# Kernel tuning notes

Hardware: AMD Instinct MI355X
Metric: run time of the kernel (lower is better)

The kernel has to match this reference:

```python
import jax, jax.numpy as jnp
import numpy as np

B, H, N, D = 4, 16, 4096, 64
M = 266  # nb_features = int(D * ln(D))
KERNEL_EPS = 1e-4


def _gaussian_orthogonal_random_matrix(nb_rows, nb_cols, rng):
    # Faithful to gaussian_orthogonal_random_matrix with scaling=0.
    blocks = []
    for _ in range(nb_rows // nb_cols):
        q, _ = np.linalg.qr(rng.standard_normal((nb_cols, nb_cols)))
        blocks.append(q.T)
    rem = nb_rows - (nb_rows // nb_cols) * nb_cols
    if rem > 0:
        q, _ = np.linalg.qr(rng.standard_normal((nb_cols, nb_cols)))
        blocks.append(q.T[:rem])
    final = np.concatenate(blocks, axis=0)
    mult = np.linalg.norm(rng.standard_normal((nb_rows, nb_cols)), axis=1)
    return (mult[:, None] * final).astype(np.float32)


def setup_inputs() -> dict:
    key = jax.random.key(0)
    kq, kk, kv = jax.random.split(key, 3)
    q = jax.random.normal(kq, (B, H, N, D), dtype=jnp.float32)
    k = jax.random.normal(kk, (B, H, N, D), dtype=jnp.float32)
    v = jax.random.normal(kv, (B, H, N, D), dtype=jnp.float32)
    proj = jnp.asarray(_gaussian_orthogonal_random_matrix(M, D, np.random.default_rng(0)))
    return {"q": q, "k": k, "v": v, "projection_matrix": proj}


def _softmax_kernel(x, proj, is_query):
    d = x.shape[-1]
    data_normalizer = d ** (-0.25)
    ratio = proj.shape[0] ** (-0.5)
    # [b,h,n,m]
    data_dash = jnp.einsum("bhnd,md->bhnm", data_normalizer * x, proj)
    diag = jnp.sum(x * x, axis=-1, keepdims=True) * 0.5 * (data_normalizer ** 2)
    if is_query:
        mx = jax.lax.stop_gradient(jnp.max(data_dash, axis=-1, keepdims=True))
    else:
        mx = jax.lax.stop_gradient(jnp.max(data_dash, axis=(-1, -2), keepdims=True))
    return ratio * (jnp.exp(data_dash - diag - mx) + KERNEL_EPS)


def _linear_attention(q, k, v):
    k_cumsum = jnp.sum(k, axis=-2)                       # [b,h,m]
    D_ = jnp.einsum("bhnm,bhm->bhn", q, k_cumsum)
    D_inv = 1.0 / jnp.where(D_ == 0, 1e-5, D_)
    context = jnp.einsum("bhnm,bhne->bhme", k, v)        # [b,h,m,e]
    return jnp.einsum("bhme,bhnm,bhn->bhne", context, q, D_inv)


def reference(q, k, v, projection_matrix):
    qp = _softmax_kernel(q, projection_matrix, is_query=True)
    kp = _softmax_kernel(k, projection_matrix, is_query=False)
    return _linear_attention(qp, kp, v)
```

## Files before the change

### kernel.cpp

```cpp
#include <hip/hip_runtime.h>
#include <math.h>


#define BH 64
#define NTOK 4096
#define DIM 64
#define MF 266
#define MPAD 272
#define NCH 4
#define CHROWS 1024
#define SUBS 16
#define RATIO 0.06131393394849658f
#define DNORM 0.35355339059327373f
#define DIAGC 0.0625f
#define KEPS 1e-4f

#define PSTR 72
#define QSTR 296

typedef _Float16 half8 __attribute__((ext_vector_type(8)));
typedef _Float16 half4 __attribute__((ext_vector_type(4)));
typedef __fp16 fp16x2 __attribute__((ext_vector_type(2)));
typedef float floatx4 __attribute__((ext_vector_type(4)));
typedef short short8 __attribute__((ext_vector_type(8)));
typedef short short4s __attribute__((ext_vector_type(4)));

__device__ __forceinline__ short f2h_bits(float f) {
    union { _Float16 h; short s; } u; u.h = (_Float16)f; return u.s;
}
__device__ __forceinline__ float h2f(short s) {
    union { short s; _Float16 h; } u; u.s = s; return (float)u.h;
}
__device__ __forceinline__ unsigned cvt_pk_bf16(float lo, float hi) {
    unsigned r;
    asm("v_cvt_pk_bf16_f32 %0, %1, %2" : "=v"(r) : "v"(lo), "v"(hi));
    return r;
}
__device__ __forceinline__ unsigned encf(float f) {
    unsigned u = __float_as_uint(f);
    return (u & 0x80000000u) ? ~u : (u | 0x80000000u);
}
__device__ __forceinline__ float decf(unsigned u) {
    u = (u & 0x80000000u) ? (u & 0x7FFFFFFFu) : ~u;
    return __uint_as_float(u);
}

__global__ __launch_bounds__(512, 4)
void k_pass(const float* __restrict__ kin, const float* __restrict__ vin,
            const float* __restrict__ proj, float* __restrict__ A0p,
            float* __restrict__ S0p, unsigned int* __restrict__ gmax)
{
    __shared__ __align__(16) short kL[2][64 * PSTR];
    __shared__ __align__(16) short vT[2][64 * PSTR];
    __shared__ float diagL[2][64];
    __shared__ __align__(16) short epS[16][16 * PSTR];

    const int tid = threadIdx.x;
    const int l = tid & 63, w = tid >> 6;
    const int c = tid & 15, g = (tid >> 4) & 3;
    const int bh = blockIdx.x >> 3;
    const int ch = (blockIdx.x >> 1) & 3;
    const int h  = blockIdx.x & 1;
    const int nT = (h == 1 && w == 0) ? 2 : 1;
    const int t0 = (h == 0) ? w : (8 + w);

    half8 pj0[2], pj1[2];
    #pragma unroll
    for (int it = 0; it < 2; ++it) {
        half8 z;
        #pragma unroll
        for (int j = 0; j < 8; ++j) z[j] = (_Float16)0.f;
        pj0[it] = z; pj1[it] = z;
        const int t = it ? 16 : t0;
        const int f = 16 * t + c;
        if (it < nT && f < MF) {
            const float* ps = proj + (size_t)f * 64 + 8 * g;
            float4 x0 = *(const float4*)ps;
            float4 x1 = *(const float4*)(ps + 4);
            float4 x2 = *(const float4*)(ps + 32);
            float4 x3 = *(const float4*)(ps + 36);
            half8 b0, b1;
            b0[0]=(_Float16)(DNORM*x0.x); b0[1]=(_Float16)(DNORM*x0.y);
            b0[2]=(_Float16)(DNORM*x0.z); b0[3]=(_Float16)(DNORM*x0.w);
            b0[4]=(_Float16)(DNORM*x1.x); b0[5]=(_Float16)(DNORM*x1.y);
            b0[6]=(_Float16)(DNORM*x1.z); b0[7]=(_Float16)(DNORM*x1.w);
            b1[0]=(_Float16)(DNORM*x2.x); b1[1]=(_Float16)(DNORM*x2.y);
            b1[2]=(_Float16)(DNORM*x2.z); b1[3]=(_Float16)(DNORM*x2.w);
            b1[4]=(_Float16)(DNORM*x3.x); b1[5]=(_Float16)(DNORM*x3.y);
            b1[6]=(_Float16)(DNORM*x3.z); b1[7]=(_Float16)(DNORM*x3.w);
            pj0[it] = b0; pj1[it] = b1;
        }
    }

    const float* kb = kin + ((size_t)bh * NTOK + (size_t)ch * CHROWS) * DIM;
    const float* vb = vin + ((size_t)bh * NTOK + (size_t)ch * CHROWS) * DIM;

    const int srow = 8 * w + (l >> 3);
    const int sd0  = (l & 7) * 8;
    const int vrow = l;
    const int ve0  = 8 * w;

    floatx4 acc[2][4];
    #pragma unroll
    for (int it = 0; it < 2; ++it)
        #pragma unroll
        for (int et = 0; et < 4; ++et) {
            acc[it][et][0]=0.f; acc[it][et][1]=0.f; acc[it][et][2]=0.f; acc[it][et][3]=0.f;
        }
    float s0acc[2] = {0.f, 0.f};
    float dmax = -3.0e38f;

    float4 ka0, ka1, va0, va1;

    auto issue_loads = [&](int s) {
        const float* ks = kb + (size_t)(64 * s + srow) * DIM + sd0;
        ka0 = *(const float4*)ks;
        ka1 = *(const float4*)(ks + 4);
        const float* vs = vb + (size_t)(64 * s + vrow) * DIM + ve0;
        va0 = *(const float4*)vs;
        va1 = *(const float4*)(vs + 4);
    };

    auto stage_write = [&](int buf) {
        union { fp16x2 h2[4]; short8 s8; } uk;
        uk.h2[0] = __builtin_amdgcn_cvt_pkrtz(ka0.x, ka0.y);
        uk.h2[1] = __builtin_amdgcn_cvt_pkrtz(ka0.z, ka0.w);
        uk.h2[2] = __builtin_amdgcn_cvt_pkrtz(ka1.x, ka1.y);
        uk.h2[3] = __builtin_amdgcn_cvt_pkrtz(ka1.z, ka1.w);
        *(short8*)&kL[buf][srow * PSTR + sd0] = uk.s8;
        float ds2 = ka0.x*ka0.x + ka0.y*ka0.y + ka0.z*ka0.z + ka0.w*ka0.w
                  + ka1.x*ka1.x + ka1.y*ka1.y + ka1.z*ka1.z + ka1.w*ka1.w;
        ds2 += __shfl_xor(ds2, 1);
        ds2 += __shfl_xor(ds2, 2);
        ds2 += __shfl_xor(ds2, 4);
        if ((l & 7) == 0) diagL[buf][srow] = ds2 * DIAGC;
        unsigned pv0 = cvt_pk_bf16(va0.x, va0.y);
        unsigned pv1 = cvt_pk_bf16(va0.z, va0.w);
        unsigned pv2 = cvt_pk_bf16(va1.x, va1.y);
        unsigned pv3 = cvt_pk_bf16(va1.z, va1.w);
        vT[buf][(ve0 + 0) * PSTR + vrow] = (short)(pv0 & 0xFFFF);
        vT[buf][(ve0 + 1) * PSTR + vrow] = (short)(pv0 >> 16);
        vT[buf][(ve0 + 2) * PSTR + vrow] = (short)(pv1 & 0xFFFF);
        vT[buf][(ve0 + 3) * PSTR + vrow] = (short)(pv1 >> 16);
        vT[buf][(ve0 + 4) * PSTR + vrow] = (short)(pv2 & 0xFFFF);
        vT[buf][(ve0 + 5) * PSTR + vrow] = (short)(pv2 >> 16);
        vT[buf][(ve0 + 6) * PSTR + vrow] = (short)(pv3 & 0xFFFF);
        vT[buf][(ve0 + 7) * PSTR + vrow] = (short)(pv3 >> 16);
    };

    issue_loads(0);
    stage_write(0);
    __syncthreads();

    for (int s = 0; s < SUBS; ++s) {
        const int cur = s & 1;
        const bool more = (s + 1 < SUBS);
        if (more) issue_loads(s + 1);

        #pragma unroll
        for (int nt = 0; nt < 4; ++nt) {
            const half8 a0 = *(const half8*)&kL[cur][(16 * nt + c) * PSTR + 8 * g];
            const half8 a1 = *(const half8*)&kL[cur][(16 * nt + c) * PSTR + 8 * g + 32];
            const float4 dg4 = *(const float4*)&diagL[cur][16 * nt + 4 * g];
            const float dgr[4] = {dg4.x, dg4.y, dg4.z, dg4.w};
            #pragma unroll
            for (int it = 0; it < 2; ++it) {
                if (it < nT) {
                    floatx4 d = {0.f, 0.f, 0.f, 0.f};
                    d = __builtin_amdgcn_mfma_f32_16x16x32_f16(a0, pj0[it], d, 0, 0, 0);
                    d = __builtin_amdgcn_mfma_f32_16x16x32_f16(a1, pj1[it], d, 0, 0, 0);
                    const bool t16 = (it == 1);
                    float ev[4];
                    #pragma unroll
                    for (int r = 0; r < 4; ++r) {
                        const float ddv = d[r];
                        if (!t16 || c < 10) dmax = fmaxf(dmax, ddv);
                        float e = __expf(ddv - dgr[r]);
                        if (t16 && c == 15) e = 1.0f;
                        s0acc[it] += e;
                        ev[r] = e;
                    }
                    uint2 pk;
                    pk.x = cvt_pk_bf16(ev[0], ev[1]);
                    pk.y = cvt_pk_bf16(ev[2], ev[3]);
                    *(uint2*)&epS[2 * w + it][c * PSTR + 16 * nt + 4 * g] = pk;
                }
            }
        }

        #pragma unroll
        for (int ntp = 0; ntp < 2; ++ntp) {
            const short8 bq0 = *(const short8*)&epS[2 * w][c * PSTR + 32 * ntp + 8 * g];
            short8 bq1;
            if (nT == 2) bq1 = *(const short8*)&epS[2 * w + 1][c * PSTR + 32 * ntp + 8 * g];
            #pragma unroll
            for (int et = 0; et < 4; ++et) {
                const short8 av = *(const short8*)&vT[cur][(16 * et + c) * PSTR + 32 * ntp + 8 * g];
                acc[0][et] = __builtin_amdgcn_mfma_f32_16x16x32_bf16(av, bq0, acc[0][et], 0, 0, 0);
                if (nT == 2)
                    acc[1][et] = __builtin_amdgcn_mfma_f32_16x16x32_bf16(av, bq1, acc[1][et], 0, 0, 0);
            }
        }

        if (more) {
            stage_write(cur ^ 1);
            __syncthreads();
        }
    }

    {
        float* dst = A0p + (size_t)(bh * NCH + ch) * (MPAD * 64);
        #pragma unroll
        for (int it = 0; it < 2; ++it) {
            if (it < nT) {
                const int t = it ? 16 : t0;
                #pragma unroll
                for (int et = 0; et < 4; ++et)
                    *(floatx4*)&dst[(size_t)(16 * t + c) * 64 + 16 * et + 4 * g] = acc[it][et];
            }
        }
    }
    #pragma unroll
    for (int it = 0; it < 2; ++it) {
        if (it < nT) {
            const int t = it ? 16 : t0;
            float s = s0acc[it];
            s += __shfl_xor(s, 16);
            s += __shfl_xor(s, 32);
            if (g == 0 && (t < 16 || c < 10))
                atomicAdd(&S0p[bh * MPAD + 16 * t + c], s);
        }
    }
    #pragma unroll
    for (int sft = 1; sft <= 32; sft <<= 1) dmax = fmaxf(dmax, __shfl_xor(dmax, sft));
    if (l == 0) atomicMax(gmax + bh, encf(dmax));
}

__global__ __launch_bounds__(512, 1)
void reduce_ctx(const float* __restrict__ A0p, const float* __restrict__ S0p,
                const unsigned int* __restrict__ gmax, short* __restrict__ ctxw)
{
    __shared__ __align__(16) short L[65 * 288];
    const int bh = blockIdx.x, tid = threadIdx.x;
    const float emx = __expf(-decf(gmax[bh]));
    const int e = tid & 63, mi = tid >> 6;
    const float* base = A0p + (size_t)bh * NCH * MPAD * 64;
    float vs = 0.f;
    #pragma unroll
    for (int c2 = 0; c2 < NCH; ++c2)
        vs += base[(size_t)c2 * MPAD * 64 + (size_t)271 * 64 + e];
    const float vsr = vs * KEPS;
    for (int m = mi; m < 288; m += 8) {
        float val = 0.f;
        if (m < MF) {
            float s = 0.f;
            #pragma unroll
            for (int c2 = 0; c2 < NCH; ++c2)
                s += base[(size_t)c2 * MPAD * 64 + (size_t)m * 64 + e];
            val = RATIO * (emx * s + vsr);
        }
        L[e * 288 + m] = f2h_bits(val);
    }
    for (int m = tid; m < 288; m += 512) {
        float val = 0.f;
        if (m < MF) val = RATIO * (emx * S0p[bh * MPAD + m] + KEPS * 4096.0f);
        L[64 * 288 + m] = f2h_bits(val);
    }
    __syncthreads();
    short* dst = ctxw + (size_t)bh * (65 * 288);
    for (int idx = tid; idx < 65 * 36; idx += 512)
        *(short8*)(dst + idx * 8) = *(const short8*)&L[idx * 8];
}

__device__ __forceinline__ void stage_proj(short* projL, const float* __restrict__ proj, int tid) {
    for (int idx = tid; idx < 544; idx += 512) {
        const int f = idx >> 1, hf = idx & 1;
        short* dst = &projL[f * PSTR + hf * 32];
        if (f < MF) {
            const float* src = proj + f * 64 + hf * 32;
            #pragma unroll
            for (int j2 = 0; j2 < 8; ++j2) {
                float4 v4 = *(const float4*)(src + j2 * 4);
                short4s sv;
                sv[0] = f2h_bits(v4.x * DNORM);
                sv[1] = f2h_bits(v4.y * DNORM);
                sv[2] = f2h_bits(v4.z * DNORM);
                sv[3] = f2h_bits(v4.w * DNORM);
                *(short4s*)(dst + j2 * 4) = sv;
            }
        } else {
            short4s z; z[0] = 0; z[1] = 0; z[2] = 0; z[3] = 0;
            #pragma unroll
            for (int j2 = 0; j2 < 8; ++j2) *(short4s*)(dst + j2 * 4) = z;
        }
    }
}

__global__ __launch_bounds__(512, 2)
void q_pass(const float* __restrict__ qin, const float* __restrict__ proj,
            const short* __restrict__ ctxw, float* __restrict__ outp)
{
    __shared__ __align__(16) short projL[MPAD * PSTR];
    __shared__ __align__(16) short ctxL[65 * QSTR];

    const int tid = threadIdx.x;
    const int bh = blockIdx.x >> 5, rt = blockIdx.x & 31;
    const int c = tid & 15, g = (tid >> 4) & 3, w = tid >> 6;

    stage_proj(projL, proj, tid);
    {
        const short* src = ctxw + (size_t)bh * (65 * 288);
        for (int idx = tid; idx < 65 * 36; idx += 512) {
            const int r = idx / 36, s = idx - r * 36;
            *(short8*)&ctxL[r * QSTR + s * 8] = *(const short8*)(src + r * 288 + s * 8);
        }
    }
    half8 bf0, bf1;
    float dsum = 0.f;
    {
        const float* qs = qin + ((size_t)bh * NTOK + rt * 128 + 16 * w + c) * DIM;
        #pragma unroll
        for (int ksi = 0; ksi < 2; ++ksi) {
            const float* p4 = qs + ksi * 32 + 8 * g;
            float4 x0 = *(const float4*)p4;
            float4 x1 = *(const float4*)(p4 + 4);
            dsum += x0.x*x0.x + x0.y*x0.y + x0.z*x0.z + x0.w*x0.w
                  + x1.x*x1.x + x1.y*x1.y + x1.z*x1.z + x1.w*x1.w;
            half8& bf = ksi ? bf1 : bf0;
            bf[0]=(_Float16)x0.x; bf[1]=(_Float16)x0.y; bf[2]=(_Float16)x0.z; bf[3]=(_Float16)x0.w;
            bf[4]=(_Float16)x1.x; bf[5]=(_Float16)x1.y; bf[6]=(_Float16)x1.z; bf[7]=(_Float16)x1.w;
        }
    }
    float t1 = dsum + __shfl_xor(dsum, 16);
    const float diagc = (t1 + __shfl_xor(t1, 32)) * DIAGC;

    __syncthreads();

    floatx4 dd[17];
    #pragma unroll
    for (int t = 0; t < 17; ++t) {
        const short* ap = &projL[(16 * t + c) * PSTR + 8 * g];
        half8 a0 = *(const half8*)ap;
        half8 a1 = *(const half8*)(ap + 32);
        floatx4 d = {0.f, 0.f, 0.f, 0.f};
        d = __builtin_amdgcn_mfma_f32_16x16x32_f16(a0, bf0, d, 0, 0, 0);
        d = __builtin_amdgcn_mfma_f32_16x16x32_f16(a1, bf1, d, 0, 0, 0);
        dd[t] = d;
    }
    float mx = -3.0e38f;
    #pragma unroll
    for (int t = 0; t < 17; ++t) {
        #pragma unroll
        for (int r2 = 0; r2 < 4; ++r2) {
            const bool fval = (t < 16) || (4 * g + r2 < 10);
            if (fval) mx = fmaxf(mx, dd[t][r2]);
        }
    }
    mx = fmaxf(mx, __shfl_xor(mx, 16));
    mx = fmaxf(mx, __shfl_xor(mx, 32));

    half4 bq[17];
    float denp = 0.f;
    #pragma unroll
    for (int t = 0; t < 17; ++t) {
        half4 b;
        #pragma unroll
        for (int r2 = 0; r2 < 4; ++r2) {
            float val = __expf(dd[t][r2] - diagc - mx) + KEPS;
            b[r2] = (_Float16)val;
            denp += val * h2f(ctxL[64 * QSTR + 16 * t + 4 * g + r2]);
        }
        bq[t] = b;
    }
    denp += __shfl_xor(denp, 16);
    denp += __shfl_xor(denp, 32);

    floatx4 acc[4];
    #pragma unroll
    for (int i = 0; i < 4; ++i) { acc[i][0]=0.f; acc[i][1]=0.f; acc[i][2]=0.f; acc[i][3]=0.f; }
    #pragma unroll
    for (int e4 = 0; e4 < 4; ++e4) {
        #pragma unroll
        for (int t = 0; t < 17; ++t) {
            half4 a4 = *(const half4*)&ctxL[(16 * e4 + c) * QSTR + 16 * t + 4 * g];
            acc[e4] = __builtin_amdgcn_mfma_f32_16x16x16f16(a4, bq[t], acc[e4], 0, 0, 0);
        }
    }
    float den = (denp == 0.f) ? 1e-5f : denp;
    const float inv = 1.0f / den;
    float* ob = outp + ((size_t)bh * NTOK + rt * 128 + 16 * w + c) * DIM;
    #pragma unroll
    for (int e4 = 0; e4 < 4; ++e4) {
        float4 o = make_float4(acc[e4][0] * inv, acc[e4][1] * inv,
                               acc[e4][2] * inv, acc[e4][3] * inv);
        *(float4*)(ob + 16 * e4 + 4 * g) = o;
    }
}

extern "C" void kernel_launch(void* const* d_in, const int* in_sizes, int n_in,
                              void* d_out, int out_size, void* d_ws, size_t ws_size,
                              hipStream_t stream)
{
    const float* q    = (const float*)d_in[0];
    const float* k    = (const float*)d_in[1];
    const float* v    = (const float*)d_in[2];
    const float* proj = (const float*)d_in[3];
    float* out = (float*)d_out;
    float* ws  = (float*)d_ws;

    const size_t offS = (size_t)BH * NCH * MPAD * 64;
    const size_t offG = offS + (size_t)BH * MPAD;
    const size_t offC = offG + 64;

    float* A0p = ws;
    float* S0p = ws + offS;
    unsigned int* gmax = (unsigned int*)(ws + offG);
    short* ctxw = (short*)(ws + offC);

    (void)hipMemsetAsync(S0p, 0, ((size_t)BH * MPAD + 64) * sizeof(float), stream);
    hipLaunchKernelGGL(k_pass, dim3(BH * NCH * 2), dim3(512), 0, stream,
                       k, v, proj, A0p, S0p, gmax);
    hipLaunchKernelGGL(reduce_ctx, dim3(BH), dim3(512), 0, stream,
                       A0p, S0p, gmax, ctxw);
    hipLaunchKernelGGL(q_pass, dim3(BH * 32), dim3(512), 0, stream,
                       q, proj, ctxw, out);
}
```

Baseline: 144.3 us.

## Precompute fp16 projection once and process two row tiles per q_pass block

The scaled fp16 projection matrix is now built once inside reduce_ctx and stored in workspace, so q_pass copies it directly instead of converting fp32 per block. q_pass blocks now loop over two 128-row tiles, halving the grid and amortising the projection and context staging across twice the rows. k_pass block indexing is reordered so the two feature-halves sit in separate grid halves. The cost is less parallelism in q_pass (1024 blocks instead of 2048) and serial work per block.

```diff
diff --git a/kernel.cpp b/kernel.cpp
--- a/kernel.cpp
+++ b/kernel.cpp
@@ -58,9 +58,10 @@
     const int tid = threadIdx.x;
     const int l = tid & 63, w = tid >> 6;
     const int c = tid & 15, g = (tid >> 4) & 3;
-    const int bh = blockIdx.x >> 3;
-    const int ch = (blockIdx.x >> 1) & 3;
-    const int h  = blockIdx.x & 1;
+    const int h    = blockIdx.x >> 8;
+    const int rest = blockIdx.x & 255;
+    const int bh   = rest >> 2;
+    const int ch   = rest & 3;
     const int nT = (h == 1 && w == 0) ? 2 : 1;
     const int t0 = (h == 0) ? w : (8 + w);
 
@@ -238,10 +239,21 @@
 
 __global__ __launch_bounds__(512, 1)
 void reduce_ctx(const float* __restrict__ A0p, const float* __restrict__ S0p,
-                const unsigned int* __restrict__ gmax, short* __restrict__ ctxw)
+                const unsigned int* __restrict__ gmax, const float* __restrict__ proj,
+                short* __restrict__ ctxw, short* __restrict__ projw)
 {
     __shared__ __align__(16) short L[65 * 288];
     const int bh = blockIdx.x, tid = threadIdx.x;
+    if (bh < 17) {
+        #pragma unroll
+        for (int rep = 0; rep < 2; ++rep) {
+            const int idx = rep * 512 + tid;
+            const int f = 16 * bh + (idx >> 6);
+            const int d = idx & 63;
+            const float val = (f < MF) ? proj[(size_t)f * 64 + d] * DNORM : 0.f;
+            projw[(size_t)f * 64 + d] = f2h_bits(val);
+        }
+    }
     const float emx = __expf(-decf(gmax[bh]));
     const int e = tid & 63, mi = tid >> 6;
     const float* base = A0p + (size_t)bh * NCH * MPAD * 64;
@@ -272,42 +284,21 @@
         *(short8*)(dst + idx * 8) = *(const short8*)&L[idx * 8];
 }
 
-__device__ __forceinline__ void stage_proj(short* projL, const float* __restrict__ proj, int tid) {
-    for (int idx = tid; idx < 544; idx += 512) {
-        const int f = idx >> 1, hf = idx & 1;
-        short* dst = &projL[f * PSTR + hf * 32];
-        if (f < MF) {
-            const float* src = proj + f * 64 + hf * 32;
-            #pragma unroll
-            for (int j2 = 0; j2 < 8; ++j2) {
-                float4 v4 = *(const float4*)(src + j2 * 4);
-                short4s sv;
-                sv[0] = f2h_bits(v4.x * DNORM);
-                sv[1] = f2h_bits(v4.y * DNORM);
-                sv[2] = f2h_bits(v4.z * DNORM);
-                sv[3] = f2h_bits(v4.w * DNORM);
-                *(short4s*)(dst + j2 * 4) = sv;
-            }
-        } else {
-            short4s z; z[0] = 0; z[1] = 0; z[2] = 0; z[3] = 0;
-            #pragma unroll
-            for (int j2 = 0; j2 < 8; ++j2) *(short4s*)(dst + j2 * 4) = z;
-        }
-    }
-}
-
 __global__ __launch_bounds__(512, 2)
-void q_pass(const float* __restrict__ qin, const float* __restrict__ proj,
+void q_pass(const float* __restrict__ qin, const short* __restrict__ projw,
             const short* __restrict__ ctxw, float* __restrict__ outp)
 {
     __shared__ __align__(16) short projL[MPAD * PSTR];
     __shared__ __align__(16) short ctxL[65 * QSTR];
 
     const int tid = threadIdx.x;
-    const int bh = blockIdx.x >> 5, rt = blockIdx.x & 31;
+    const int bh = blockIdx.x >> 4, rt = blockIdx.x & 15;
     const int c = tid & 15, g = (tid >> 4) & 3, w = tid >> 6;
 
-    stage_proj(projL, proj, tid);
+    for (int idx = tid; idx < MPAD * 8; idx += 512) {
+        const int r = idx >> 3, s = idx & 7;
+        *(short8*)&projL[r * PSTR + s * 8] = *(const short8*)(projw + (size_t)r * 64 + s * 8);
+    }
     {
         const short* src = ctxw + (size_t)bh * (65 * 288);
         for (int idx = tid; idx < 65 * 36; idx += 512) {
@@ -315,85 +306,88 @@
             *(short8*)&ctxL[r * QSTR + s * 8] = *(const short8*)(src + r * 288 + s * 8);
         }
     }
-    half8 bf0, bf1;
-    float dsum = 0.f;
-    {
-        const float* qs = qin + ((size_t)bh * NTOK + rt * 128 + 16 * w + c) * DIM;
-        #pragma unroll
-        for (int ksi = 0; ksi < 2; ++ksi) {
-            const float* p4 = qs + ksi * 32 + 8 * g;
-            float4 x0 = *(const float4*)p4;
-            float4 x1 = *(const float4*)(p4 + 4);
-            dsum += x0.x*x0.x + x0.y*x0.y + x0.z*x0.z + x0.w*x0.w
-                  + x1.x*x1.x + x1.y*x1.y + x1.z*x1.z + x1.w*x1.w;
-            half8& bf = ksi ? bf1 : bf0;
-            bf[0]=(_Float16)x0.x; bf[1]=(_Float16)x0.y; bf[2]=(_Float16)x0.z; bf[3]=(_Float16)x0.w;
-            bf[4]=(_Float16)x1.x; bf[5]=(_Float16)x1.y; bf[6]=(_Float16)x1.z; bf[7]=(_Float16)x1.w;
-        }
-    }
-    float t1 = dsum + __shfl_xor(dsum, 16);
-    const float diagc = (t1 + __shfl_xor(t1, 32)) * DIAGC;
-
     __syncthreads();
 
-    floatx4 dd[17];
-    #pragma unroll
-    for (int t = 0; t < 17; ++t) {
-        const short* ap = &projL[(16 * t + c) * PSTR + 8 * g];
-        half8 a0 = *(const half8*)ap;
-        half8 a1 = *(const half8*)(ap + 32);
-        floatx4 d = {0.f, 0.f, 0.f, 0.f};
-        d = __builtin_amdgcn_mfma_f32_16x16x32_f16(a0, bf0, d, 0, 0, 0);
-        d = __builtin_amdgcn_mfma_f32_16x16x32_f16(a1, bf1, d, 0, 0, 0);
-        dd[t] = d;
-    }
-    float mx = -3.0e38f;
-    #pragma unroll
-    for (int t = 0; t < 17; ++t) {
-        #pragma unroll
-        for (int r2 = 0; r2 < 4; ++r2) {
-            const bool fval = (t < 16) || (4 * g + r2 < 10);
-            if (fval) mx = fmaxf(mx, dd[t][r2]);
-        }
-    }
-    mx = fmaxf(mx, __shfl_xor(mx, 16));
-    mx = fmaxf(mx, __shfl_xor(mx, 32));
-
-    half4 bq[17];
-    float denp = 0.f;
-    #pragma unroll
-    for (int t = 0; t < 17; ++t) {
-        half4 b;
-        #pragma unroll
-        for (int r2 = 0; r2 < 4; ++r2) {
-            float val = __expf(dd[t][r2] - diagc - mx) + KEPS;
-            b[r2] = (_Float16)val;
-            denp += val * h2f(ctxL[64 * QSTR + 16 * t + 4 * g + r2]);
-        }
-        bq[t] = b;
-    }
-    denp += __shfl_xor(denp, 16);
-    denp += __shfl_xor(denp, 32);
-
-    floatx4 acc[4];
-    #pragma unroll
-    for (int i = 0; i < 4; ++i) { acc[i][0]=0.f; acc[i][1]=0.f; acc[i][2]=0.f; acc[i][3]=0.f; }
-    #pragma unroll
-    for (int e4 = 0; e4 < 4; ++e4) {
+    for (int rg = 0; rg < 2; ++rg) {
+        const int rowbase = rt * 256 + rg * 128;
+        half8 bf0, bf1;
+        float dsum = 0.f;
+        {
+            const float* qs = qin + ((size_t)bh * NTOK + rowbase + 16 * w + c) * DIM;
+            #pragma unroll
+            for (int ksi = 0; ksi < 2; ++ksi) {
+                const float* p4 = qs + ksi * 32 + 8 * g;
+                float4 x0 = *(const float4*)p4;
+                float4 x1 = *(const float4*)(p4 + 4);
+                dsum += x0.x*x0.x + x0.y*x0.y + x0.z*x0.z + x0.w*x0.w
+                      + x1.x*x1.x + x1.y*x1.y + x1.z*x1.z + x1.w*x1.w;
+                half8& bf = ksi ? bf1 : bf0;
+                bf[0]=(_Float16)x0.x; bf[1]=(_Float16)x0.y; bf[2]=(_Float16)x0.z; bf[3]=(_Float16)x0.w;
+                bf[4]=(_Float16)x1.x; bf[5]=(_Float16)x1.y; bf[6]=(_Float16)x1.z; bf[7]=(_Float16)x1.w;
+            }
+        }
+        float t1 = dsum + __shfl_xor(dsum, 16);
+        const float diagc = (t1 + __shfl_xor(t1, 32)) * DIAGC;
+
+        floatx4 dd[17];
         #pragma unroll
         for (int t = 0; t < 17; ++t) {
-            half4 a4 = *(const half4*)&ctxL[(16 * e4 + c) * QSTR + 16 * t + 4 * g];
-            acc[e4] = __builtin_amdgcn_mfma_f32_16x16x16f16(a4, bq[t], acc[e4], 0, 0, 0);
-        }
-    }
-    float den = (denp == 0.f) ? 1e-5f : denp;
-    const float inv = 1.0f / den;
-    float* ob = outp + ((size_t)bh * NTOK + rt * 128 + 16 * w + c) * DIM;
-    #pragma unroll
-    for (int e4 = 0; e4 < 4; ++e4) {
-        float4 o = make_float4(acc[e4][0] * inv, acc[e4][1] * inv,
-                               acc[e4][2] * inv, acc[e4][3] * inv);
-        *(float4*)(ob + 16 * e4 + 4 * g) = o;
+            const short* ap = &projL[(16 * t + c) * PSTR + 8 * g];
+            half8 a0 = *(const half8*)ap;
+            half8 a1 = *(const half8*)(ap + 32);
+            floatx4 d = {0.f, 0.f, 0.f, 0.f};
+            d = __builtin_amdgcn_mfma_f32_16x16x32_f16(a0, bf0, d, 0, 0, 0);
+            d = __builtin_amdgcn_mfma_f32_16x16x32_f16(a1, bf1, d, 0, 0, 0);
+            dd[t] = d;
+        }
+        float mx = -3.0e38f;
+        #pragma unroll
+        for (int t = 0; t < 17; ++t) {
+            #pragma unroll
+            for (int r2 = 0; r2 < 4; ++r2) {
+                const bool fval = (t < 16) || (4 * g + r2 < 10);
+                if (fval) mx = fmaxf(mx, dd[t][r2]);
+            }
+        }
+        mx = fmaxf(mx, __shfl_xor(mx, 16));
+        mx = fmaxf(mx, __shfl_xor(mx, 32));
+
+        half4 bq[17];
+        float denp = 0.f;
+        #pragma unroll
+        for (int t = 0; t < 17; ++t) {
+            half4 b;
+            #pragma unroll
+            for (int r2 = 0; r2 < 4; ++r2) {
+                float val = __expf(dd[t][r2] - diagc - mx) + KEPS;
+                b[r2] = (_Float16)val;
+                denp += val * h2f(ctxL[64 * QSTR + 16 * t + 4 * g + r2]);
+            }
+            bq[t] = b;
+        }
+        denp += __shfl_xor(denp, 16);
+        denp += __shfl_xor(denp, 32);
+
+        floatx4 acc[4];
+        #pragma unroll
+        for (int i = 0; i < 4; ++i) { acc[i][0]=0.f; acc[i][1]=0.f; acc[i][2]=0.f; acc[i][3]=0.f; }
+        #pragma unroll
+        for (int e4 = 0; e4 < 4; ++e4) {
+            #pragma unroll
+            for (int t = 0; t < 17; ++t) {
+                half4 a4 = *(const half4*)&ctxL[(16 * e4 + c) * QSTR + 16 * t + 4 * g];
+                acc[e4] = __builtin_amdgcn_mfma_f32_16x16x16f16(a4, bq[t], acc[e4], 0, 0, 0);
+            }
+        }
+        float den = (denp == 0.f) ? 1e-5f : denp;
+        const float inv = 1.0f / den;
+        float* ob = outp + ((size_t)bh * NTOK + rowbase + 16 * w + c) * DIM;
+        #pragma unroll
+        for (int e4 = 0; e4 < 4; ++e4) {
+            float4 o = make_float4(acc[e4][0] * inv, acc[e4][1] * inv,
+                                   acc[e4][2] * inv, acc[e4][3] * inv);
+            *(float4*)(ob + 16 * e4 + 4 * g) = o;
+        }
     }
 }
 
@@ -411,17 +405,19 @@
     const size_t offS = (size_t)BH * NCH * MPAD * 64;
     const size_t offG = offS + (size_t)BH * MPAD;
     const size_t offC = offG + 64;
+    const size_t offP = offC + (size_t)BH * 65 * 288 / 2;
 
     float* A0p = ws;
     float* S0p = ws + offS;
     unsigned int* gmax = (unsigned int*)(ws + offG);
     short* ctxw = (short*)(ws + offC);
+    short* projw = (short*)(ws + offP);
 
     (void)hipMemsetAsync(S0p, 0, ((size_t)BH * MPAD + 64) * sizeof(float), stream);
     hipLaunchKernelGGL(k_pass, dim3(BH * NCH * 2), dim3(512), 0, stream,
                        k, v, proj, A0p, S0p, gmax);
     hipLaunchKernelGGL(reduce_ctx, dim3(BH), dim3(512), 0, stream,
-                       A0p, S0p, gmax, ctxw);
-    hipLaunchKernelGGL(q_pass, dim3(BH * 32), dim3(512), 0, stream,
-                       q, proj, ctxw, out);
-}
+                       A0p, S0p, gmax, proj, ctxw, projw);
+    hipLaunchKernelGGL(q_pass, dim3(BH * 16), dim3(512), 0, stream,
+                       q, projw, ctxw, out);
+}
```

Result: slower. 322.3 us (+123.4%).
